# Optimization experiments

Measured on AMD Instinct MI355X. Metric: run time of the kernel, lower is better.

The kernel has to match this reference:

```python
import jax, jax.numpy as jnp
import numpy as np
from jax import lax

RATES = (2, 3, 5, 9)
C_IN = 64
B, H, W = 4, 128, 128


def conv2d(x, w, b, dilation):
    # x: [B,C,H,W], w: [O,I,3,3]; padding=dilation keeps spatial size
    y = lax.conv_general_dilated(
        x, w, window_strides=(1, 1),
        padding=[(dilation, dilation), (dilation, dilation)],
        rhs_dilation=(dilation, dilation),
        dimension_numbers=('NCHW', 'OIHW', 'NCHW'))
    return y + b[None, :, None, None]


def bilinear_sample(x, py, px):
    # x: [B,C,H,W]; py,px: [B,K,H,W] float sampling positions; zeros outside
    Hh, Ww = x.shape[-2], x.shape[-1]
    y0 = jnp.floor(py)
    x0 = jnp.floor(px)
    wy1 = py - y0
    wx1 = px - x0
    wy0 = 1.0 - wy1
    wx0 = 1.0 - wx1

    def gather(yi, xi):
        valid = (yi >= 0) & (yi < Hh) & (xi >= 0) & (xi < Ww)
        yc = jnp.clip(yi, 0, Hh - 1).astype(jnp.int32)
        xc = jnp.clip(xi, 0, Ww - 1).astype(jnp.int32)
        # per-batch fancy gather: [C,K,H,W]
        vals = jax.vmap(lambda im, yy, xx: im[:, yy, xx])(x, yc, xc)
        return vals * valid[:, None].astype(x.dtype)

    out = (gather(y0, x0) * (wy0 * wx0)[:, None]
           + gather(y0, x0 + 1) * (wy0 * wx1)[:, None]
           + gather(y0 + 1, x0) * (wy1 * wx0)[:, None]
           + gather(y0 + 1, x0 + 1) * (wy1 * wx1)[:, None])
    return out  # [B,C,K,H,W]


def deform_conv(x, offset, weight, dilation):
    # offset: [B,18,H,W] = (dy,dx) per kernel point; weight: [O,C,3,3]
    b, c, h, w = x.shape
    K = 9
    off = offset.reshape(b, K, 2, h, w)
    dy, dx = off[:, :, 0], off[:, :, 1]
    ky = jnp.repeat((jnp.arange(3) - 1) * dilation, 3).astype(x.dtype)  # [9]
    kx = jnp.tile((jnp.arange(3) - 1) * dilation, 3).astype(x.dtype)
    hh = jnp.arange(h, dtype=x.dtype)[None, None, :, None]
    ww = jnp.arange(w, dtype=x.dtype)[None, None, None, :]
    py = hh + ky[None, :, None, None] + dy
    px = ww + kx[None, :, None, None] + dx
    sampled = bilinear_sample(x, py, px)  # [B,C,K,H,W]
    w9 = weight.reshape(weight.shape[0], c, K)
    return jnp.einsum('bckhw,ock->bohw', sampled, w9)


def setup_inputs() -> dict:
    key = jax.random.key(0)
    ks = jax.random.split(key, 8)
    s = 0.05
    return {
        'x': jax.random.normal(ks[0], (B, C_IN, H, W), jnp.float32),
        'dw': jax.random.normal(ks[1], (4, C_IN, C_IN, 3, 3), jnp.float32) * s,
        'ow': jax.random.normal(ks[2], (4, 18, C_IN, 3, 3), jnp.float32) * s,
        'ob': jax.random.normal(ks[3], (4, 18), jnp.float32) * s,
        'se_w1': jax.random.normal(ks[4], (C_IN, 4 * C_IN), jnp.float32) * s,
        'se_b1': jax.random.normal(ks[5], (C_IN,), jnp.float32) * s,
        'se_w2': jax.random.normal(ks[6], (4 * C_IN, C_IN), jnp.float32) * s,
        'se_b2': jax.random.normal(ks[7], (4 * C_IN,), jnp.float32) * s,
    }


def reference(x, dw, ow, ob, se_w1, se_b1, se_w2, se_b2):
    b, c, h, w = x.shape
    outs = []
    for i in range(4):
        j = (i - 1) % 4  # faithful to `self.offsets[i - 1]` in the source
        off = jax.nn.relu(conv2d(x, ow[j], ob[j], RATES[j]))
        outs.append(deform_conv(x, off, dw[i], RATES[i]))
    cat = jnp.concatenate(outs, axis=1)  # [B,4C,H,W]
    # SENet on concatenated features
    g = cat.mean(axis=(2, 3))  # [B,4C]
    h1 = jax.nn.relu(g @ se_w1.T + se_b1)
    s = jax.nn.sigmoid(h1 @ se_w2.T + se_b2)  # [B,4C]
    gated = (1.0 + s)[:, :, None, None] * cat
    fused = gated.reshape(b, 4, c, h, w).sum(axis=1)  # sum over the 4 stages
    return x + fused
```

## Files before the change

kernel.cpp:

```cpp
#include <hip/hip_runtime.h>
#include <hip/hip_bf16.h>
#include <math.h>

#define BATCH 4
#define CIN 64
#define HH 128
#define WW 128
#define HWP (HH*WW)

#define OFF_OFF   0
#define CAT_OFF   4718592
#define XBF_OFF   (CAT_OFF + 8388608)
#define XHWC_OFF  (XBF_OFF + 2097152)
#define WTB_OFF   (CAT_OFF + 16777216)
#define OWT_OFF   (WTB_OFF + 147456)
#define G_OFF     (OWT_OFF + 41472)
#define SCALE_OFF (G_OFF + 1024)

typedef __attribute__((ext_vector_type(8))) short short8;
typedef __attribute__((ext_vector_type(8))) unsigned short ushort8;
typedef __attribute__((ext_vector_type(4))) float f32x4;

__device__ __forceinline__ int rate_of(int i) {
    return (i == 0) ? 2 : (i == 1) ? 3 : (i == 2) ? 5 : 9;
}

__device__ __forceinline__ short f2bf(float f) {
    union { float f; unsigned u; } v; v.f = f;
    unsigned u = v.u + 0x7FFFu + ((v.u >> 16) & 1u);
    return (short)(u >> 16);
}
__device__ __forceinline__ float bf2f(unsigned short u) {
    union { unsigned u; float f; } v; v.u = ((unsigned)u) << 16;
    return v.f;
}

__global__ __launch_bounds__(256) void prep_kernel(
    const float* __restrict__ x,  const float* __restrict__ dw,
    const float* __restrict__ ow, unsigned short* __restrict__ xbf,
    short* __restrict__ wtb, float* __restrict__ owT)
{
    int idx = blockIdx.x * 256 + threadIdx.x;
    if (idx < 4194304) {
        xbf[idx] = (unsigned short)f2bf(x[idx]);
        return;
    }
    int idx1 = idx - 4194304;
    if (idx1 < 147456) {
        int c = idx1 & 63;
        int k = (idx1 >> 6) % 9;
        int r = idx1 / 576;
        int o = r & 63;
        int i = r >> 6;
        wtb[idx1] = f2bf(dw[((i * 64 + o) * 64 + c) * 9 + k]);
        return;
    }
    int idx2 = idx1 - 147456;
    if (idx2 < 41472) {
        int o = idx2 % 18;
        int r = idx2 / 18;
        int tap = r % 9; r /= 9;
        int c = r & 63;
        int j = r >> 6;
        owT[idx2] = ow[((j * 18 + o) * 64 + c) * 9 + tap];
    }
}

__global__ __launch_bounds__(256) void xhwc_kernel(
    const float* __restrict__ x, unsigned short* __restrict__ xhwc)
{
    const int t  = threadIdx.x;
    const int b  = blockIdx.y;
    const int p0 = blockIdx.x * 64;
    const int px = t & 63;
    const int cO = t >> 6;

    const float* xb = x + (size_t)b * CIN * HWP + p0 + px;
    unsigned short* xh = xhwc + ((size_t)b * HWP + p0 + px) * 64;

#pragma unroll
    for (int g = 0; g < 2; ++g) {
        const int cb = cO * 8 + g * 32;
        ushort8 v;
#pragma unroll
        for (int cj = 0; cj < 8; ++cj)
            v[cj] = (unsigned short)f2bf(xb[(size_t)(cb + cj) * HWP]);
        *(ushort8*)(xh + cb) = v;
    }
}

__global__ __launch_bounds__(256) void offset_conv_kernel(
    const unsigned short* __restrict__ xbf, const float* __restrict__ owT,
    const float* __restrict__ ob, float* __restrict__ off)
{
    const int t  = threadIdx.x;
    const int lx = t & 63, ly = t >> 6;
    const int w0 = blockIdx.x * 64 + lx;
    const int h0 = blockIdx.y * 4 + ly;
    const int z  = blockIdx.z;
    const int j  = z >> 2, b = z & 3;
    const int d  = rate_of(j);

    int addr[9]; float msk[9];
#pragma unroll
    for (int tap = 0; tap < 9; ++tap) {
        const int iy = tap / 3, ix = tap % 3;
        const int xx = w0 + (ix - 1) * d;
        const int yy = h0 + (iy - 1) * d;
        const bool v = ((unsigned)xx < (unsigned)WW) && ((unsigned)yy < (unsigned)HH);
        addr[tap] = min(max(yy, 0), HH - 1) * WW + min(max(xx, 0), WW - 1);
        msk[tap]  = v ? 1.f : 0.f;
    }

    float acc[18];
#pragma unroll
    for (int o = 0; o < 18; ++o) acc[o] = ob[j * 18 + o];

    const unsigned short* xb = xbf + (size_t)b * CIN * HWP;
    float p[9];
#pragma unroll
    for (int tap = 0; tap < 9; ++tap) p[tap] = bf2f(xb[addr[tap]]);

    for (int c = 0; c < CIN; ++c) {
        const unsigned short* xn = xb + (c < CIN - 1 ? c + 1 : CIN - 1) * HWP;
        float q[9];
#pragma unroll
        for (int tap = 0; tap < 9; ++tap) q[tap] = bf2f(xn[addr[tap]]);

        const float* wp = owT + ((j * 64 + c) * 9) * 18;
#pragma unroll
        for (int tap = 0; tap < 9; ++tap) {
            const float v = p[tap] * msk[tap];
            const float* wt = wp + tap * 18;
#pragma unroll
            for (int o = 0; o < 18; ++o)
                acc[o] = fmaf(v, wt[o], acc[o]);
        }
#pragma unroll
        for (int tap = 0; tap < 9; ++tap) p[tap] = q[tap];
    }

    float* op = off + (size_t)z * 18 * HWP + h0 * WW + w0;
#pragma unroll
    for (int o = 0; o < 18; ++o) op[o * HWP] = fmaxf(acc[o], 0.f);
}

__global__ __launch_bounds__(256) void deform_mfma_kernel(
    const unsigned short* __restrict__ xhwc, const short* __restrict__ wtb,
    const float* __restrict__ off, unsigned short* __restrict__ cat)
{
    __shared__ __align__(16) short S[2][64][72];

    const int t  = threadIdx.x;
    const int z  = blockIdx.y;
    const int i  = z >> 2, b = z & 3;
    const int d  = rate_of(i);
    const int j  = (i + 3) & 3;
    const int ty = blockIdx.x >> 1;
    const int tx = blockIdx.x & 1;

    const int spx = t & 127;
    const int cg  = t >> 7;
    const int sly = spx >> 6, slx = spx & 63;
    const int ph  = ty * 2 + sly, pw = tx * 64 + slx;
    const int pg  = ph * WW + pw;

    const int wv = t >> 6, lane = t & 63;
    const int nl = lane & 15, quad = lane >> 4;

    const unsigned short* xh = xhwc + (size_t)b * HWP * 64;
    const float* offp = off + ((size_t)(j * 4 + b) * 18) * HWP + pg;

    f32x4 acc[8];
#pragma unroll
    for (int nt = 0; nt < 8; ++nt) acc[nt] = (f32x4){0.f, 0.f, 0.f, 0.f};

    for (int k = 0; k < 9; ++k) {
        const int iy = k / 3, ix = k % 3;
        float dy = offp[(2 * k) * HWP];
        float dx = offp[(2 * k + 1) * HWP];
        float py = (float)(ph + (iy - 1) * d) + dy;
        float px = (float)(pw + (ix - 1) * d) + dx;
        float fy0 = floorf(py), fx0 = floorf(px);
        float wy1 = py - fy0, wx1 = px - fx0;
        float wy0 = 1.f - wy1, wx0 = 1.f - wx1;
        int y0 = (int)fy0, x0 = (int)fx0;
        int y1 = y0 + 1,  x1 = x0 + 1;
        bool vy0 = (unsigned)y0 < (unsigned)HH, vy1 = (unsigned)y1 < (unsigned)HH;
        bool vx0 = (unsigned)x0 < (unsigned)WW, vx1 = (unsigned)x1 < (unsigned)WW;
        int yc0 = min(max(y0, 0), HH - 1), yc1 = min(max(y1, 0), HH - 1);
        int xc0 = min(max(x0, 0), WW - 1), xc1 = min(max(x1, 0), WW - 1);
        float w00 = (vy0 && vx0) ? wy0 * wx0 : 0.f;
        float w01 = (vy0 && vx1) ? wy0 * wx1 : 0.f;
        float w10 = (vy1 && vx0) ? wy1 * wx0 : 0.f;
        float w11 = (vy1 && vx1) ? wy1 * wx1 : 0.f;
        const unsigned short* pc00 = xh + (size_t)(yc0 * WW + xc0) * 64;
        const unsigned short* pc01 = xh + (size_t)(yc0 * WW + xc1) * 64;
        const unsigned short* pc10 = xh + (size_t)(yc1 * WW + xc0) * 64;
        const unsigned short* pc11 = xh + (size_t)(yc1 * WW + xc1) * 64;

        if (k) __syncthreads();

#pragma unroll
        for (int ch = 0; ch < 4; ++ch) {
            const int cb = cg * 32 + ch * 8;
            ushort8 u00 = *(const ushort8*)(pc00 + cb);
            ushort8 u01 = *(const ushort8*)(pc01 + cb);
            ushort8 u10 = *(const ushort8*)(pc10 + cb);
            ushort8 u11 = *(const ushort8*)(pc11 + cb);
            short8 pk;
#pragma unroll
            for (int cj = 0; cj < 8; ++cj) {
                float v = bf2f(u00[cj]) * w00 + bf2f(u01[cj]) * w01
                        + bf2f(u10[cj]) * w10 + bf2f(u11[cj]) * w11;
                pk[cj] = f2bf(v);
            }
            *(__shared__ short8*)&S[sly][slx][cb] = pk;
        }
        __syncthreads();

        const short* wrow = wtb + ((size_t)((i * 64 + wv * 16 + nl) * 9 + k)) * 64;
#pragma unroll
        for (int q2 = 0; q2 < 2; ++q2) {
            short8 a = *(const short8*)&wrow[q2 * 32 + quad * 8];
#pragma unroll
            for (int nt = 0; nt < 8; ++nt) {
                short8 bfr = *(const __shared__ short8*)
                    &S[nt >> 2][(nt & 3) * 16 + nl][q2 * 32 + quad * 8];
                acc[nt] = __builtin_amdgcn_mfma_f32_16x16x32_bf16(a, bfr, acc[nt], 0, 0, 0);
            }
        }
    }

#pragma unroll
    for (int nt = 0; nt < 8; ++nt) {
        const int prow = ty * 2 + (nt >> 2);
        const int pcol = tx * 64 + (nt & 3) * 16 + nl;
        unsigned short* cp = cat
            + ((size_t)(b * 256 + i * 64 + wv * 16 + quad * 4)) * HWP
            + prow * WW + pcol;
#pragma unroll
        for (int r = 0; r < 4; ++r)
            cp[(size_t)r * HWP] = (unsigned short)f2bf(acc[nt][r]);
    }
}

__global__ __launch_bounds__(256) void reduce_kernel(
    const unsigned short* __restrict__ cat, float* __restrict__ g)
{
    const int bc = blockIdx.x;
    const unsigned short* p = cat + (size_t)bc * HWP;
    float s = 0.f;
#pragma unroll
    for (int q = 0; q < 8; ++q) {
        short8 v8 = *(const short8*)(p + q * 2048 + threadIdx.x * 8);
#pragma unroll
        for (int e = 0; e < 8; ++e) s += bf2f((unsigned short)v8[e]);
    }
#pragma unroll
    for (int o = 32; o > 0; o >>= 1) s += __shfl_down(s, o, 64);
    __shared__ float ls[4];
    if ((threadIdx.x & 63) == 0) ls[threadIdx.x >> 6] = s;
    __syncthreads();
    if (threadIdx.x == 0) {
        g[bc] = (ls[0] + ls[1] + ls[2] + ls[3]) * (1.f / (float)HWP);
    }
}

__global__ __launch_bounds__(256) void se_kernel(
    const float* __restrict__ g,  const float* __restrict__ w1,
    const float* __restrict__ b1, const float* __restrict__ w2,
    const float* __restrict__ b2, float* __restrict__ scale)
{
    __shared__ float gs[1024];
    __shared__ float h1s[256];
    const int t = threadIdx.x;
#pragma unroll
    for (int q = 0; q < 4; ++q) gs[q * 256 + t] = g[q * 256 + t];
    __syncthreads();
    {
        int b = t >> 6, o = t & 63;
        float a = b1[o];
        for (int c = 0; c < 256; ++c)
            a = fmaf(gs[b * 256 + c], w1[o * 256 + c], a);
        h1s[t] = fmaxf(a, 0.f);
    }
    __syncthreads();
#pragma unroll
    for (int q = 0; q < 4; ++q) {
        int idx = q * 256 + t;
        int b = idx >> 8, cc = idx & 255;
        float a = b2[cc];
#pragma unroll 8
        for (int o = 0; o < 64; ++o)
            a = fmaf(h1s[b * 64 + o], w2[cc * 64 + o], a);
        scale[idx] = 1.f + 1.f / (1.f + expf(-a));
    }
}

__global__ __launch_bounds__(256) void final_kernel(
    const float* __restrict__ x, const unsigned short* __restrict__ cat,
    const float* __restrict__ scale, float* __restrict__ out)
{
    const int gid = blockIdx.x;
    const int p = (gid & 63) * 256 + threadIdx.x;
    const int c = (gid >> 6) & 63;
    const int b = gid >> 12;
    const float s0 = scale[b * 256 + c];
    const float s1 = scale[b * 256 + 64 + c];
    const float s2 = scale[b * 256 + 128 + c];
    const float s3 = scale[b * 256 + 192 + c];
    const unsigned short* cb = cat + ((size_t)(b * 256 + c)) * HWP + p;
    float v = x[(size_t)(b * 64 + c) * HWP + p];
    v = fmaf(s0, bf2f(cb[0 * 64 * HWP]), v);
    v = fmaf(s1, bf2f(cb[1 * 64 * HWP]), v);
    v = fmaf(s2, bf2f(cb[2 * 64 * HWP]), v);
    v = fmaf(s3, bf2f(cb[3 * 64 * HWP]), v);
    out[(size_t)(b * 64 + c) * HWP + p] = v;
}

extern "C" void kernel_launch(void* const* d_in, const int* in_sizes, int n_in,
                              void* d_out, int out_size, void* d_ws, size_t ws_size,
                              hipStream_t stream) {
    const float* x  = (const float*)d_in[0];
    const float* dw = (const float*)d_in[1];
    const float* ow = (const float*)d_in[2];
    const float* ob = (const float*)d_in[3];
    const float* w1 = (const float*)d_in[4];
    const float* b1 = (const float*)d_in[5];
    const float* w2 = (const float*)d_in[6];
    const float* b2 = (const float*)d_in[7];
    float* out = (float*)d_out;
    float* ws  = (float*)d_ws;

    float* OFF            = ws + OFF_OFF;
    unsigned short* CAT   = (unsigned short*)(ws + CAT_OFF);
    unsigned short* XBF   = (unsigned short*)(ws + XBF_OFF);
    unsigned short* XHWC  = (unsigned short*)(ws + XHWC_OFF);
    short* WTB            = (short*)(ws + WTB_OFF);
    float* OWT            = ws + OWT_OFF;
    float* G              = ws + G_OFF;
    float* SCALE          = ws + SCALE_OFF;

    prep_kernel<<<17122, 256, 0, stream>>>(x, dw, ow, XBF, WTB, OWT);
    xhwc_kernel<<<dim3(256, 4), 256, 0, stream>>>(x, XHWC);
    offset_conv_kernel<<<dim3(2, 32, 16), 256, 0, stream>>>(XBF, OWT, ob, OFF);
    deform_mfma_kernel<<<dim3(128, 16), 256, 0, stream>>>(XHWC, WTB, OFF, CAT);
    reduce_kernel<<<1024, 256, 0, stream>>>(CAT, G);
    se_kernel<<<1, 256, 0, stream>>>(G, w1, b1, w2, b2, SCALE);
    final_kernel<<<16384, 256, 0, stream>>>(x, CAT, SCALE, out);
}
```

Measured before the change: 366.1 us.

## Remap deform gather threads to 8 channel chunks per pixel and swap MFMA tile ownership

The bilinear gather now assigns eight threads per pixel, each loading one 16-byte channel chunk, so a pixel's 128-byte channel vector is read contiguously by adjacent lanes instead of being split across two thread groups. Each wave now owns 32 pixels across all 64 output channels rather than 16 output channels across all pixels. B fragments come from LDS once per q2 and A weight rows are loaded per M tile from global memory. The aim is better coalescing of the gathers and fewer LDS reads, at the cost of recomputing the offset and bilinear weight maths eight times per pixel and issuing more global weight loads.

```diff
diff --git a/kernel.cpp b/kernel.cpp
--- a/kernel.cpp
+++ b/kernel.cpp
@@ -149,7 +149,7 @@
     const unsigned short* __restrict__ xhwc, const short* __restrict__ wtb,
     const float* __restrict__ off, unsigned short* __restrict__ cat)
 {
-    __shared__ __align__(16) short S[2][64][72];
+    __shared__ __align__(16) short S[128][72];
 
     const int t  = threadIdx.x;
     const int z  = blockIdx.y;
@@ -159,55 +159,55 @@
     const int ty = blockIdx.x >> 1;
     const int tx = blockIdx.x & 1;
 
-    const int spx = t & 127;
-    const int cg  = t >> 7;
-    const int sly = spx >> 6, slx = spx & 63;
-    const int ph  = ty * 2 + sly, pw = tx * 64 + slx;
-    const int pg  = ph * WW + pw;
+    const int chunk = t & 7;
+    const int pxb   = t >> 3;
 
     const int wv = t >> 6, lane = t & 63;
     const int nl = lane & 15, quad = lane >> 4;
 
     const unsigned short* xh = xhwc + (size_t)b * HWP * 64;
-    const float* offp = off + ((size_t)(j * 4 + b) * 18) * HWP + pg;
+    const float* offb = off + ((size_t)(j * 4 + b) * 18) * HWP;
 
     f32x4 acc[8];
 #pragma unroll
-    for (int nt = 0; nt < 8; ++nt) acc[nt] = (f32x4){0.f, 0.f, 0.f, 0.f};
+    for (int a = 0; a < 8; ++a) acc[a] = (f32x4){0.f, 0.f, 0.f, 0.f};
 
     for (int k = 0; k < 9; ++k) {
         const int iy = k / 3, ix = k % 3;
-        float dy = offp[(2 * k) * HWP];
-        float dx = offp[(2 * k + 1) * HWP];
-        float py = (float)(ph + (iy - 1) * d) + dy;
-        float px = (float)(pw + (ix - 1) * d) + dx;
-        float fy0 = floorf(py), fx0 = floorf(px);
-        float wy1 = py - fy0, wx1 = px - fx0;
-        float wy0 = 1.f - wy1, wx0 = 1.f - wx1;
-        int y0 = (int)fy0, x0 = (int)fx0;
-        int y1 = y0 + 1,  x1 = x0 + 1;
-        bool vy0 = (unsigned)y0 < (unsigned)HH, vy1 = (unsigned)y1 < (unsigned)HH;
-        bool vx0 = (unsigned)x0 < (unsigned)WW, vx1 = (unsigned)x1 < (unsigned)WW;
-        int yc0 = min(max(y0, 0), HH - 1), yc1 = min(max(y1, 0), HH - 1);
-        int xc0 = min(max(x0, 0), WW - 1), xc1 = min(max(x1, 0), WW - 1);
-        float w00 = (vy0 && vx0) ? wy0 * wx0 : 0.f;
-        float w01 = (vy0 && vx1) ? wy0 * wx1 : 0.f;
-        float w10 = (vy1 && vx0) ? wy1 * wx0 : 0.f;
-        float w11 = (vy1 && vx1) ? wy1 * wx1 : 0.f;
-        const unsigned short* pc00 = xh + (size_t)(yc0 * WW + xc0) * 64;
-        const unsigned short* pc01 = xh + (size_t)(yc0 * WW + xc1) * 64;
-        const unsigned short* pc10 = xh + (size_t)(yc1 * WW + xc0) * 64;
-        const unsigned short* pc11 = xh + (size_t)(yc1 * WW + xc1) * 64;
 
         if (k) __syncthreads();
 
 #pragma unroll
-        for (int ch = 0; ch < 4; ++ch) {
-            const int cb = cg * 32 + ch * 8;
-            ushort8 u00 = *(const ushort8*)(pc00 + cb);
-            ushort8 u01 = *(const ushort8*)(pc01 + cb);
-            ushort8 u10 = *(const ushort8*)(pc10 + cb);
-            ushort8 u11 = *(const ushort8*)(pc11 + cb);
+        for (int it = 0; it < 4; ++it) {
+            const int psub = it * 32 + pxb;
+            const int sly = psub >> 6, slx = psub & 63;
+            const int ph = ty * 2 + sly, pw = tx * 64 + slx;
+            const int pg = ph * WW + pw;
+
+            float dy = offb[(2 * k) * HWP + pg];
+            float dx = offb[(2 * k + 1) * HWP + pg];
+            float py = (float)(ph + (iy - 1) * d) + dy;
+            float px = (float)(pw + (ix - 1) * d) + dx;
+            float fy0 = floorf(py), fx0 = floorf(px);
+            float wy1 = py - fy0, wx1 = px - fx0;
+            float wy0 = 1.f - wy1, wx0 = 1.f - wx1;
+            int y0 = (int)fy0, x0 = (int)fx0;
+            int y1 = y0 + 1,  x1 = x0 + 1;
+            bool vy0 = (unsigned)y0 < (unsigned)HH, vy1 = (unsigned)y1 < (unsigned)HH;
+            bool vx0 = (unsigned)x0 < (unsigned)WW, vx1 = (unsigned)x1 < (unsigned)WW;
+            int yc0 = min(max(y0, 0), HH - 1), yc1 = min(max(y1, 0), HH - 1);
+            int xc0 = min(max(x0, 0), WW - 1), xc1 = min(max(x1, 0), WW - 1);
+            float w00 = (vy0 && vx0) ? wy0 * wx0 : 0.f;
+            float w01 = (vy0 && vx1) ? wy0 * wx1 : 0.f;
+            float w10 = (vy1 && vx0) ? wy1 * wx0 : 0.f;
+            float w11 = (vy1 && vx1) ? wy1 * wx1 : 0.f;
+
+            const int cb = chunk * 8;
+            ushort8 u00 = *(const ushort8*)(xh + (size_t)(yc0 * WW + xc0) * 64 + cb);
+            ushort8 u01 = *(const ushort8*)(xh + (size_t)(yc0 * WW + xc1) * 64 + cb);
+            ushort8 u10 = *(const ushort8*)(xh + (size_t)(yc1 * WW + xc0) * 64 + cb);
+            ushort8 u11 = *(const ushort8*)(xh + (size_t)(yc1 * WW + xc1) * 64 + cb);
+
             short8 pk;
 #pragma unroll
             for (int cj = 0; cj < 8; ++cj) {
@@ -215,33 +215,40 @@
                         + bf2f(u10[cj]) * w10 + bf2f(u11[cj]) * w11;
                 pk[cj] = f2bf(v);
             }
-            *(__shared__ short8*)&S[sly][slx][cb] = pk;
+            *(__shared__ short8*)&S[psub][cb] = pk;
         }
         __syncthreads();
 
-        const short* wrow = wtb + ((size_t)((i * 64 + wv * 16 + nl) * 9 + k)) * 64;
 #pragma unroll
         for (int q2 = 0; q2 < 2; ++q2) {
-            short8 a = *(const short8*)&wrow[q2 * 32 + quad * 8];
-#pragma unroll
-            for (int nt = 0; nt < 8; ++nt) {
-                short8 bfr = *(const __shared__ short8*)
-                    &S[nt >> 2][(nt & 3) * 16 + nl][q2 * 32 + quad * 8];
-                acc[nt] = __builtin_amdgcn_mfma_f32_16x16x32_bf16(a, bfr, acc[nt], 0, 0, 0);
+            short8 b0 = *(const __shared__ short8*)&S[wv * 32 + nl][q2 * 32 + quad * 8];
+            short8 b1 = *(const __shared__ short8*)&S[wv * 32 + 16 + nl][q2 * 32 + quad * 8];
+#pragma unroll
+            for (int mt = 0; mt < 4; ++mt) {
+                const short* wrow = wtb
+                    + ((size_t)((i * 64 + mt * 16 + nl) * 9 + k)) * 64;
+                short8 a = *(const short8*)&wrow[q2 * 32 + quad * 8];
+                acc[mt * 2 + 0] = __builtin_amdgcn_mfma_f32_16x16x32_bf16(a, b0, acc[mt * 2 + 0], 0, 0, 0);
+                acc[mt * 2 + 1] = __builtin_amdgcn_mfma_f32_16x16x32_bf16(a, b1, acc[mt * 2 + 1], 0, 0, 0);
             }
         }
     }
 
 #pragma unroll
-    for (int nt = 0; nt < 8; ++nt) {
-        const int prow = ty * 2 + (nt >> 2);
-        const int pcol = tx * 64 + (nt & 3) * 16 + nl;
-        unsigned short* cp = cat
-            + ((size_t)(b * 256 + i * 64 + wv * 16 + quad * 4)) * HWP
-            + prow * WW + pcol;
-#pragma unroll
-        for (int r = 0; r < 4; ++r)
-            cp[(size_t)r * HWP] = (unsigned short)f2bf(acc[nt][r]);
+    for (int mt = 0; mt < 4; ++mt) {
+#pragma unroll
+        for (int nt = 0; nt < 2; ++nt) {
+            const int psub = wv * 32 + nt * 16 + nl;
+            const int prow = ty * 2 + (psub >> 6);
+            const int pcol = tx * 64 + (psub & 63);
+            unsigned short* cp = cat
+                + ((size_t)(b * 256 + i * 64 + mt * 16 + quad * 4)) * HWP
+                + prow * WW + pcol;
+            const f32x4 v = acc[mt * 2 + nt];
+#pragma unroll
+            for (int r = 0; r < 4; ++r)
+                cp[(size_t)r * HWP] = (unsigned short)f2bf(v[r]);
+        }
     }
 }
 
```

Result: faster. 342.1 us (-6.6%).
